# Performance work log

Measured on AMD Instinct MI355X. Metric: run time of the kernel, lower is better.

The kernel has to match this reference:

```python
import jax, jax.numpy as jnp
import numpy as np
from jax.ops import segment_sum

N_NODES = 50000
N_EDGES = 150000
IN_FEATS = 512
OUT_FEATS = 512


def setup_inputs() -> dict:
    key = jax.random.key(0)
    k1, k2, k3, k4 = jax.random.split(key, 4)
    x = jax.random.normal(k1, (N_NODES, IN_FEATS), dtype=jnp.float32)
    src = jax.random.randint(k2, (N_EDGES,), 0, N_NODES, dtype=jnp.int64)
    dst = jax.random.randint(k3, (N_EDGES,), 0, N_NODES, dtype=jnp.int64)
    # Xavier-uniform init like reset_parameters
    limit = float(np.sqrt(6.0 / (IN_FEATS + OUT_FEATS)))
    W = jax.random.uniform(k4, (IN_FEATS, OUT_FEATS), dtype=jnp.float32,
                           minval=-limit, maxval=limit)
    b = jnp.zeros((OUT_FEATS,), dtype=jnp.float32)
    return {"x": x, "src": src, "dst": dst, "W": W, "b": b}


def reference(x, src, dst, W, b):
    # DGL GraphConv with norm='both':
    #   out = relu( D_dst^{-1/2} A D_src^{-1/2} X W + b )
    # Dropout is identity in eval mode (training=False).
    ones = jnp.ones((src.shape[0],), dtype=x.dtype)
    deg_out = segment_sum(ones, src, num_segments=N_NODES)  # source out-degree
    deg_in = segment_sum(ones, dst, num_segments=N_NODES)   # dest in-degree
    norm_src = jnp.where(deg_out > 0, deg_out, 1.0) ** -0.5  # [N]
    norm_dst = jnp.where(deg_in > 0, deg_in, 1.0) ** -0.5    # [N]

    h = x * norm_src[:, None]                         # [N, in]
    agg = segment_sum(h[src], dst, num_segments=N_NODES)  # scatter-add over edges
    agg = agg * norm_dst[:, None]                     # [N, in]
    out = agg @ W + b                                 # [N, out]
    return jax.nn.relu(out)
```

## Files before the change

kernel.cpp:

```cpp
#include <hip/hip_runtime.h>
#include <hip/hip_bf16.h>

#define N_NODES 50000
#define N_PAD   50048
#define N_EDGES 150000
#define F 512
#define BM 128
#define BN 128
#define BK 64
#define NBLK 196
#define NWG  1564

typedef __attribute__((ext_vector_type(4))) float f32x4;
typedef __attribute__((ext_vector_type(4))) unsigned int u32x4;
typedef __attribute__((ext_vector_type(2))) unsigned int u32x2;

__device__ __forceinline__ unsigned short f2bf(float f) {
    unsigned int u = __float_as_uint(f);
    return (unsigned short)((u + 0x7fffu + ((u >> 16) & 1u)) >> 16);
}
__device__ __forceinline__ unsigned int pack2(float a, float b) {
    return (unsigned int)f2bf(a) | ((unsigned int)f2bf(b) << 16);
}
__device__ __forceinline__ void gload16(const void* g, void* l) {
    __builtin_amdgcn_global_load_lds(
        (const __attribute__((address_space(1))) unsigned int*)g,
        (__attribute__((address_space(3))) unsigned int*)l, 16, 0, 0);
}

__global__ void __launch_bounds__(256) crd_deg(const int* __restrict__ src,
                                               const int* __restrict__ dst,
                                               int* __restrict__ hist) {
    int e = blockIdx.x * 256 + threadIdx.x;
    if (e < N_EDGES) {
        atomicAdd(&hist[src[e]], 1);
        atomicAdd(&hist[N_NODES + dst[e]], 1);
    }
}

__global__ void __launch_bounds__(256) crd_norm(const int* __restrict__ hist,
                                                float* __restrict__ norms) {
    int i = blockIdx.x * 256 + threadIdx.x;
    if (i < 2 * N_NODES) {
        int d = hist[i];
        norms[i] = rsqrtf((float)(d > 0 ? d : 1));
    }
}

__global__ void __launch_bounds__(256) crd_bsum(const int* __restrict__ hist_in,
                                                int* __restrict__ bsum) {
    __shared__ int s[256];
    int t = threadIdx.x;
    int i = blockIdx.x * 256 + t;
    s[t] = (i < N_NODES) ? hist_in[i] : 0;
    __syncthreads();
    #pragma unroll
    for (int o = 128; o > 0; o >>= 1) {
        if (t < o) s[t] += s[t + o];
        __syncthreads();
    }
    if (t == 0) bsum[blockIdx.x] = s[0];
}

__global__ void __launch_bounds__(256) crd_bscan(const int* __restrict__ bsum,
                                                 int* __restrict__ bsumoff) {
    __shared__ int s[256];
    int t = threadIdx.x;
    int v = (t < NBLK) ? bsum[t] : 0;
    s[t] = v;
    __syncthreads();
    #pragma unroll
    for (int d = 1; d < 256; d <<= 1) {
        int add = (t >= d) ? s[t - d] : 0;
        __syncthreads();
        s[t] += add;
        __syncthreads();
    }
    if (t < NBLK) bsumoff[t] = s[t] - v;
}

__global__ void __launch_bounds__(256) crd_escan(const int* __restrict__ hist_in,
                                                 const int* __restrict__ bsumoff,
                                                 int* __restrict__ off,
                                                 int* __restrict__ cursor) {
    __shared__ int s[256];
    int t = threadIdx.x;
    int i = blockIdx.x * 256 + t;
    int v = (i < N_NODES) ? hist_in[i] : 0;
    s[t] = v;
    __syncthreads();
    #pragma unroll
    for (int d = 1; d < 256; d <<= 1) {
        int add = (t >= d) ? s[t - d] : 0;
        __syncthreads();
        s[t] += add;
        __syncthreads();
    }
    int excl = s[t] - v + bsumoff[blockIdx.x];
    if (i < N_NODES) { off[i] = excl; cursor[i] = excl; }
    if (i == N_NODES - 1) off[N_NODES] = excl + v;
}

__global__ void __launch_bounds__(256) crd_place(const int* __restrict__ src,
                                                 const int* __restrict__ dst,
                                                 int* __restrict__ cursor,
                                                 int* __restrict__ sorted) {
    int e = blockIdx.x * 256 + threadIdx.x;
    if (e < N_EDGES) {
        int slot = atomicAdd(&cursor[dst[e]], 1);
        sorted[slot] = src[e];
    }
}

__global__ void __launch_bounds__(256) crd_wt(const float* __restrict__ W,
                                              unsigned short* __restrict__ Wt) {
    int idx = blockIdx.x * 256 + threadIdx.x;
    int n = idx >> 9, k = idx & 511;
    Wt[idx] = f2bf(W[k * F + n]);
}

__global__ void __launch_bounds__(256) crd_gather(const float* __restrict__ x,
                                                  const int* __restrict__ sorted,
                                                  const int* __restrict__ off,
                                                  const float* __restrict__ norms,
                                                  unsigned short* __restrict__ aggb) {
    int wid = (blockIdx.x * 256 + threadIdx.x) >> 6;
    int lane = threadIdx.x & 63;
    if (wid >= N_PAD) return;
    f32x4 a0 = {0.f,0.f,0.f,0.f}, a1 = a0, b0 = a0, b1 = a0;
    if (wid < N_NODES) {
        int e0 = off[wid], e1 = off[wid + 1];
        int e = e0;
        for (; e + 1 < e1; e += 2) {
            int s0 = sorted[e], s1 = sorted[e + 1];
            float ns0 = norms[s0], ns1 = norms[s1];
            const f32x4* p0 = (const f32x4*)(x + (size_t)s0 * F);
            const f32x4* p1 = (const f32x4*)(x + (size_t)s1 * F);
            a0 += p0[lane] * ns0;  a1 += p0[64 + lane] * ns0;
            b0 += p1[lane] * ns1;  b1 += p1[64 + lane] * ns1;
        }
        if (e < e1) {
            int s = sorted[e];
            float ns = norms[s];
            const f32x4* p = (const f32x4*)(x + (size_t)s * F);
            a0 += p[lane] * ns;  a1 += p[64 + lane] * ns;
        }
        float nd = norms[N_NODES + wid];
        a0 = (a0 + b0) * nd;
        a1 = (a1 + b1) * nd;
    }
    unsigned short* row = aggb + (size_t)wid * F;
    u32x2 w0, w1;
    w0.x = pack2(a0.x, a0.y); w0.y = pack2(a0.z, a0.w);
    w1.x = pack2(a1.x, a1.y); w1.y = pack2(a1.z, a1.w);
    *(u32x2*)(row + lane * 4) = w0;
    *(u32x2*)(row + 256 + lane * 4) = w1;
}

__global__ void __launch_bounds__(256, 3) crd_gemm(const unsigned short* __restrict__ aggb,
                                                   const unsigned short* __restrict__ Wt,
                                                   const float* __restrict__ bias,
                                                   float* __restrict__ out) {
    __shared__ __align__(16) unsigned short lA[8 * BM * 8];
    __shared__ __align__(16) unsigned short lB[8 * BN * 8];
    const int tid = threadIdx.x;
    int bid = blockIdx.x;
    int xcd = bid & 7, lid = bid >> 3;
    int swz = (xcd < 4 ? xcd * 196 : 784 + (xcd - 4) * 195) + lid;
    const int rowbase = (swz >> 2) * BM;
    const int nbase = (swz & 3) * BN;
    const int lane = tid & 63;
    const int wave = tid >> 6;
    const int wm = wave >> 1, wn = wave & 1;
    const int g = lane >> 4, r = lane & 15;

    f32x4 acc[4][4];
    #pragma unroll
    for (int i = 0; i < 4; ++i)
        #pragma unroll
        for (int j = 0; j < 4; ++j) acc[i][j] = (f32x4){0.f, 0.f, 0.f, 0.f};

    for (int ks = 0; ks < F / BK; ++ks) {
        #pragma unroll
        for (int j = 0; j < 4; ++j) {
            int gg = (wave * 4 + j) * 64 + lane;
            int k8 = gg >> 7, row = gg & 127;
            gload16(aggb + (size_t)(rowbase + row) * F + ks * BK + k8 * 8,
                    &lA[(size_t)(wave * 4 + j) * 64 * 8]);
        }
        #pragma unroll
        for (int j = 0; j < 4; ++j) {
            int gg = (wave * 4 + j) * 64 + lane;
            int k8 = gg >> 7, n = gg & 127;
            gload16(Wt + (size_t)(nbase + n) * F + ks * BK + k8 * 8,
                    &lB[(size_t)(wave * 4 + j) * 64 * 8]);
        }
        __syncthreads();
        #pragma unroll
        for (int kk = 0; kk < 2; ++kk) {
            int k8 = kk * 4 + g;
            u32x4 af[4], bfr[4];
            #pragma unroll
            for (int mi = 0; mi < 4; ++mi)
                af[mi] = *(const u32x4*)&lA[(k8 * BM + wm * 64 + mi * 16 + r) * 8];
            #pragma unroll
            for (int ni = 0; ni < 4; ++ni)
                bfr[ni] = *(const u32x4*)&lB[(k8 * BN + wn * 64 + ni * 16 + r) * 8];
            #pragma unroll
            for (int mi = 0; mi < 4; ++mi)
                #pragma unroll
                for (int ni = 0; ni < 4; ++ni)
                    asm("v_mfma_f32_16x16x32_bf16 %0, %1, %2, %0"
                        : "+v"(acc[mi][ni]) : "v"(bfr[ni]), "v"(af[mi]));
        }
        __syncthreads();
    }
    #pragma unroll
    for (int mi = 0; mi < 4; ++mi) {
        int row = rowbase + wm * 64 + mi * 16 + r;
        if (row < N_NODES) {
            #pragma unroll
            for (int ni = 0; ni < 4; ++ni) {
                int c0 = nbase + wn * 64 + ni * 16 + g * 4;
                f32x4 bv = *(const f32x4*)(bias + c0);
                f32x4 v = acc[mi][ni] + bv;
                v.x = v.x > 0.f ? v.x : 0.f;
                v.y = v.y > 0.f ? v.y : 0.f;
                v.z = v.z > 0.f ? v.z : 0.f;
                v.w = v.w > 0.f ? v.w : 0.f;
                *(f32x4*)(out + (size_t)row * F + c0) = v;
            }
        }
    }
}

extern "C" void kernel_launch(void* const* d_in, const int* in_sizes, int n_in,
                              void* d_out, int out_size, void* d_ws, size_t ws_size,
                              hipStream_t stream) {
    const float* x = (const float*)d_in[0];
    const int* src = (const int*)d_in[1];
    const int* dst = (const int*)d_in[2];
    const float* W = (const float*)d_in[3];
    const float* bias = (const float*)d_in[4];
    float* out = (float*)d_out;

    unsigned short* aggb = (unsigned short*)d_ws;
    unsigned short* Wt = aggb + (size_t)N_PAD * F;
    float* norms = (float*)(Wt + (size_t)F * F);
    int* hist = (int*)(norms + 2 * N_NODES);
    int* off = hist + 2 * N_NODES;
    int* cursor = off + N_NODES + 1;
    int* sorted = cursor + N_NODES;
    int* bsum = sorted + N_EDGES;
    int* bsumoff = bsum + NBLK;
    size_t need = (size_t)((char*)(bsumoff + NBLK) - (char*)d_ws);
    if (ws_size < need) {
        hipMemsetAsync(d_out, 0, (size_t)out_size * sizeof(float), stream);
        return;
    }

    hipMemsetAsync(hist, 0, 2 * N_NODES * sizeof(int), stream);
    crd_deg<<<(N_EDGES + 255) / 256, 256, 0, stream>>>(src, dst, hist);
    crd_norm<<<(2 * N_NODES + 255) / 256, 256, 0, stream>>>(hist, norms);
    crd_bsum<<<NBLK, 256, 0, stream>>>(hist + N_NODES, bsum);
    crd_bscan<<<1, 256, 0, stream>>>(bsum, bsumoff);
    crd_escan<<<NBLK, 256, 0, stream>>>(hist + N_NODES, bsumoff, off, cursor);
    crd_wt<<<(F * F) / 256, 256, 0, stream>>>(W, Wt);
    crd_place<<<(N_EDGES + 255) / 256, 256, 0, stream>>>(src, dst, cursor, sorted);
    crd_gather<<<N_PAD / 4, 256, 0, stream>>>(x, sorted, off, norms, aggb);
    crd_gemm<<<NWG, 256, 0, stream>>>(aggb, Wt, bias, out);
}
```

Before: 165.9 us.

## Reorder to GEMM-then-aggregate with bf16 pre-scaled features and fused epilogue

Uses associativity to compute H = (D_src^{-1/2} X) W first and then aggregate H rows per destination node. A new kernel pre-scales X by the source norm and converts it to bf16. The GEMM writes bf16 H, and a new gather kernel sums neighbour rows of H and applies the destination norm, bias and ReLU. The goal is to make the random per-edge gather read a smaller bf16 table instead of fp32 X rows. In exchange it adds a full pass over X, an extra bf16 rounding of H before summation, and a dependency on a larger workspace, with the old path kept as a fallback.

```diff
diff --git a/kernel.cpp b/kernel.cpp
--- a/kernel.cpp
+++ b/kernel.cpp
@@ -117,6 +117,69 @@
     int idx = blockIdx.x * 256 + threadIdx.x;
     int n = idx >> 9, k = idx & 511;
     Wt[idx] = f2bf(W[k * F + n]);
+}
+
+__global__ void __launch_bounds__(256) crd_xb(const float* __restrict__ x,
+                                              const float* __restrict__ norms,
+                                              unsigned short* __restrict__ xb) {
+    int t = blockIdx.x * 256 + threadIdx.x;
+    size_t i = (size_t)t * 8;
+    float ns = norms[t >> 6];
+    f32x4 v0 = *(const f32x4*)(x + i);
+    f32x4 v1 = *(const f32x4*)(x + i + 4);
+    v0 *= ns; v1 *= ns;
+    u32x4 w;
+    w.x = pack2(v0.x, v0.y); w.y = pack2(v0.z, v0.w);
+    w.z = pack2(v1.x, v1.y); w.w = pack2(v1.z, v1.w);
+    *(u32x4*)(xb + i) = w;
+}
+
+__device__ __forceinline__ void acc8(float* a, u32x4 v) {
+    a[0] += __uint_as_float(v.x << 16); a[1] += __uint_as_float(v.x & 0xffff0000u);
+    a[2] += __uint_as_float(v.y << 16); a[3] += __uint_as_float(v.y & 0xffff0000u);
+    a[4] += __uint_as_float(v.z << 16); a[5] += __uint_as_float(v.z & 0xffff0000u);
+    a[6] += __uint_as_float(v.w << 16); a[7] += __uint_as_float(v.w & 0xffff0000u);
+}
+
+__global__ void __launch_bounds__(256) crd_gout(const unsigned short* __restrict__ H,
+                                                const int* __restrict__ sorted,
+                                                const int* __restrict__ off,
+                                                const float* __restrict__ norms,
+                                                const float* __restrict__ bias,
+                                                float* __restrict__ out) {
+    int wid = (blockIdx.x * 256 + threadIdx.x) >> 6;
+    int lane = threadIdx.x & 63;
+    if (wid >= N_NODES) return;
+    float a[8] = {0.f,0.f,0.f,0.f,0.f,0.f,0.f,0.f};
+    float b[8] = {0.f,0.f,0.f,0.f,0.f,0.f,0.f,0.f};
+    int e0 = off[wid], e1 = off[wid + 1];
+    int e = e0;
+    for (; e + 1 < e1; e += 2) {
+        int s0 = sorted[e], s1 = sorted[e + 1];
+        u32x4 v0 = *(const u32x4*)(H + (size_t)s0 * F + lane * 8);
+        u32x4 v1 = *(const u32x4*)(H + (size_t)s1 * F + lane * 8);
+        acc8(a, v0);
+        acc8(b, v1);
+    }
+    if (e < e1) {
+        u32x4 v = *(const u32x4*)(H + (size_t)sorted[e] * F + lane * 8);
+        acc8(a, v);
+    }
+    float nd = norms[N_NODES + wid];
+    f32x4 bv0 = *(const f32x4*)(bias + lane * 8);
+    f32x4 bv1 = *(const f32x4*)(bias + lane * 8 + 4);
+    f32x4 o0, o1;
+    o0.x = fmaxf((a[0] + b[0]) * nd + bv0.x, 0.f);
+    o0.y = fmaxf((a[1] + b[1]) * nd + bv0.y, 0.f);
+    o0.z = fmaxf((a[2] + b[2]) * nd + bv0.z, 0.f);
+    o0.w = fmaxf((a[3] + b[3]) * nd + bv0.w, 0.f);
+    o1.x = fmaxf((a[4] + b[4]) * nd + bv1.x, 0.f);
+    o1.y = fmaxf((a[5] + b[5]) * nd + bv1.y, 0.f);
+    o1.z = fmaxf((a[6] + b[6]) * nd + bv1.z, 0.f);
+    o1.w = fmaxf((a[7] + b[7]) * nd + bv1.w, 0.f);
+    float* po = out + (size_t)wid * F + lane * 8;
+    *(f32x4*)po = o0;
+    *(f32x4*)(po + 4) = o1;
 }
 
 __global__ void __launch_bounds__(256) crd_gather(const float* __restrict__ x,
@@ -157,10 +220,11 @@
     *(u32x2*)(row + 256 + lane * 4) = w1;
 }
 
-__global__ void __launch_bounds__(256, 3) crd_gemm(const unsigned short* __restrict__ aggb,
+template <int TO_BF16>
+__global__ void __launch_bounds__(256, 3) crd_gemm(const unsigned short* __restrict__ A,
                                                    const unsigned short* __restrict__ Wt,
                                                    const float* __restrict__ bias,
-                                                   float* __restrict__ out) {
+                                                   void* __restrict__ outp) {
     __shared__ __align__(16) unsigned short lA[8 * BM * 8];
     __shared__ __align__(16) unsigned short lB[8 * BN * 8];
     const int tid = threadIdx.x;
@@ -185,7 +249,7 @@
         for (int j = 0; j < 4; ++j) {
             int gg = (wave * 4 + j) * 64 + lane;
             int k8 = gg >> 7, row = gg & 127;
-            gload16(aggb + (size_t)(rowbase + row) * F + ks * BK + k8 * 8,
+            gload16(A + (size_t)(rowbase + row) * F + ks * BK + k8 * 8,
                     &lA[(size_t)(wave * 4 + j) * 64 * 8]);
         }
         #pragma unroll
@@ -218,16 +282,25 @@
     #pragma unroll
     for (int mi = 0; mi < 4; ++mi) {
         int row = rowbase + wm * 64 + mi * 16 + r;
-        if (row < N_NODES) {
+        if (TO_BF16) {
+            unsigned short* H = (unsigned short*)outp;
+            #pragma unroll
+            for (int ni = 0; ni < 4; ++ni) {
+                int c0 = nbase + wn * 64 + ni * 16 + g * 4;
+                u32x2 w;
+                w.x = pack2(acc[mi][ni].x, acc[mi][ni].y);
+                w.y = pack2(acc[mi][ni].z, acc[mi][ni].w);
+                *(u32x2*)(H + (size_t)row * F + c0) = w;
+            }
+        } else if (row < N_NODES) {
+            float* out = (float*)outp;
             #pragma unroll
             for (int ni = 0; ni < 4; ++ni) {
                 int c0 = nbase + wn * 64 + ni * 16 + g * 4;
                 f32x4 bv = *(const f32x4*)(bias + c0);
                 f32x4 v = acc[mi][ni] + bv;
-                v.x = v.x > 0.f ? v.x : 0.f;
-                v.y = v.y > 0.f ? v.y : 0.f;
-                v.z = v.z > 0.f ? v.z : 0.f;
-                v.w = v.w > 0.f ? v.w : 0.f;
+                v.x = fmaxf(v.x, 0.f); v.y = fmaxf(v.y, 0.f);
+                v.z = fmaxf(v.z, 0.f); v.w = fmaxf(v.w, 0.f);
                 *(f32x4*)(out + (size_t)row * F + c0) = v;
             }
         }
@@ -244,29 +317,40 @@
     const float* bias = (const float*)d_in[4];
     float* out = (float*)d_out;
 
-    unsigned short* aggb = (unsigned short*)d_ws;
-    unsigned short* Wt = aggb + (size_t)N_PAD * F;
-    float* norms = (float*)(Wt + (size_t)F * F);
+    float* norms = (float*)d_ws;
     int* hist = (int*)(norms + 2 * N_NODES);
     int* off = hist + 2 * N_NODES;
     int* cursor = off + N_NODES + 1;
     int* sorted = cursor + N_NODES;
     int* bsum = sorted + N_EDGES;
     int* bsumoff = bsum + NBLK;
-    size_t need = (size_t)((char*)(bsumoff + NBLK) - (char*)d_ws);
-    if (ws_size < need) {
+    unsigned short* Wt = (unsigned short*)
+        (((uintptr_t)(bsumoff + NBLK) + 63) & ~(uintptr_t)63);
+    unsigned short* xb = Wt + (size_t)F * F;
+    unsigned short* H  = xb + (size_t)N_PAD * F;
+    size_t need_min = (size_t)((char*)(xb + (size_t)N_PAD * F) - (char*)d_ws);
+    size_t need_big = (size_t)((char*)(H  + (size_t)N_PAD * F) - (char*)d_ws);
+    if (ws_size < need_min) {
         hipMemsetAsync(d_out, 0, (size_t)out_size * sizeof(float), stream);
         return;
     }
+    const bool reorder = (ws_size >= need_big);
 
     hipMemsetAsync(hist, 0, 2 * N_NODES * sizeof(int), stream);
     crd_deg<<<(N_EDGES + 255) / 256, 256, 0, stream>>>(src, dst, hist);
     crd_norm<<<(2 * N_NODES + 255) / 256, 256, 0, stream>>>(hist, norms);
+    crd_wt<<<(F * F) / 256, 256, 0, stream>>>(W, Wt);
     crd_bsum<<<NBLK, 256, 0, stream>>>(hist + N_NODES, bsum);
     crd_bscan<<<1, 256, 0, stream>>>(bsum, bsumoff);
     crd_escan<<<NBLK, 256, 0, stream>>>(hist + N_NODES, bsumoff, off, cursor);
-    crd_wt<<<(F * F) / 256, 256, 0, stream>>>(W, Wt);
     crd_place<<<(N_EDGES + 255) / 256, 256, 0, stream>>>(src, dst, cursor, sorted);
-    crd_gather<<<N_PAD / 4, 256, 0, stream>>>(x, sorted, off, norms, aggb);
-    crd_gemm<<<NWG, 256, 0, stream>>>(aggb, Wt, bias, out);
-}
+
+    if (reorder) {
+        crd_xb<<<(int)(((size_t)N_NODES * F / 8) / 256), 256, 0, stream>>>(x, norms, xb);
+        crd_gemm<1><<<NWG, 256, 0, stream>>>(xb, Wt, bias, H);
+        crd_gout<<<N_NODES * 64 / 256, 256, 0, stream>>>(H, sorted, off, norms, bias, out);
+    } else {
+        crd_gather<<<N_PAD / 4, 256, 0, stream>>>(x, sorted, off, norms, xb);
+        crd_gemm<0><<<NWG, 256, 0, stream>>>(xb, Wt, bias, out);
+    }
+}
```

Measured after the change: 180.8 us. +9.0%, slower.
